# Optimization experiments

Measured on AMD Instinct MI355X. Metric: run time of the kernel, lower is better.

Reference implementation:

```python
import jax, jax.numpy as jnp
import numpy as np

NH = 8          # number of attention heads
RAND_P = 0.1    # random attention probability
EPS = 1e-5      # LayerNorm eps (torch default)


def _layer_norm(x, g, b):
    m = x.mean(-1, keepdims=True)
    v = ((x - m) ** 2).mean(-1, keepdims=True)
    return (x - m) * jax.lax.rsqrt(v + EPS) * g + b


def _make_mask(u, n_frames, spatial):
    # random(0/1) + tiled-eye position mask + block-diagonal frame mask (additive float mask)
    L = n_frames * spatial
    idx = jnp.arange(L)
    frame_id = idx // spatial
    pos_id = idx % spatial
    rand = (u >= RAND_P).astype(jnp.float32)
    pos = (pos_id[:, None] == pos_id[None, :]).astype(jnp.float32)
    frame = (frame_id[:, None] == frame_id[None, :]).astype(jnp.float32)
    return rand + pos + frame  # [L, L], values in {0,1,2,3}


def _attn_block(f, u, Wqkv, bqkv, Wo, bo, g1, b1, Wfc1, bfc1, Wfc2, bfc2, g2, b2):
    N, C, H, W = f.shape
    S = H * W
    L = N * S
    hd = C // NH
    src = f.transpose(0, 2, 3, 1).reshape(L, C)  # (n,h,w) flatten order, batch=1 squeezed
    mask = _make_mask(u, N, S)

    qkv = src @ Wqkv.T + bqkv                    # [L, 3C]
    q, k, v = jnp.split(qkv, 3, axis=-1)
    q = q.reshape(L, NH, hd).transpose(1, 0, 2) * (hd ** -0.5)  # [H, L, hd]
    k = k.reshape(L, NH, hd).transpose(1, 0, 2)
    v = v.reshape(L, NH, hd).transpose(1, 0, 2)

    scores = jnp.einsum('hqd,hkd->hqk', q, k) + mask[None]      # [H, L, L]
    attn = jax.nn.softmax(scores, axis=-1)
    o = jnp.einsum('hqk,hkd->hqd', attn, v).transpose(1, 0, 2).reshape(L, C)
    src2 = o @ Wo.T + bo

    x = _layer_norm(src + src2, g1, b1)          # residual + LN (dropout p=0 -> identity)
    h = jax.nn.relu(x @ Wfc1.T + bfc1)
    x = _layer_norm(x + h @ Wfc2.T + bfc2, g2, b2)
    return x.reshape(N, H, W, C).transpose(0, 3, 1, 2)


def setup_inputs() -> dict:
    key = jax.random.key(0)
    ks = jax.random.split(key, 12)
    D = 256
    s = 0.02
    return {
        'f0': jax.random.normal(ks[0], (2, D, 80, 80), jnp.float32),
        'f1': jax.random.normal(ks[1], (2, D, 40, 40), jnp.float32),
        'f2': jax.random.normal(ks[2], (2, D, 32, 32), jnp.float32),
        'f3': jax.random.normal(ks[3], (2, D, 16, 16), jnp.float32),
        'u2': jax.random.uniform(ks[4], (2048, 2048), jnp.float32),
        'u3': jax.random.uniform(ks[5], (512, 512), jnp.float32),
        'Wqkv': jax.random.normal(ks[6], (3 * D, D), jnp.float32) * s,
        'bqkv': jnp.zeros((3 * D,), jnp.float32),
        'Wo': jax.random.normal(ks[7], (D, D), jnp.float32) * s,
        'bo': jnp.zeros((D,), jnp.float32),
        'g1': jnp.ones((D,), jnp.float32),
        'b1': jnp.zeros((D,), jnp.float32),
        'Wfc1': jax.random.normal(ks[8], (4 * D, D), jnp.float32) * s,
        'bfc1': jnp.zeros((4 * D,), jnp.float32),
        'Wfc2': jax.random.normal(ks[9], (D, 4 * D), jnp.float32) * s,
        'bfc2': jnp.zeros((D,), jnp.float32),
        'g2': jnp.ones((D,), jnp.float32),
        'b2': jnp.zeros((D,), jnp.float32),
    }


def reference(f0, f1, f2, f3, u2, u3, Wqkv, bqkv, Wo, bo, g1, b1,
              Wfc1, bfc1, Wfc2, bfc2, g2, b2):
    params = (Wqkv, bqkv, Wo, bo, g1, b1, Wfc1, bfc1, Wfc2, bfc2, g2, b2)
    # levels 0 and 1 pass through untouched (loop starts at i=2)
    out2 = _attn_block(f2, u2, *params)
    out3 = _attn_block(f3, u3, *params)
    return (f0, f1, out2, out3)
```

## Files before the change

kernel.cpp:

```cpp
#include <hip/hip_runtime.h>
#include <hip/hip_bf16.h>
#include <cstddef>


typedef __attribute__((ext_vector_type(8))) short s16x8;
typedef __attribute__((ext_vector_type(4))) short s16x4;
typedef __attribute__((ext_vector_type(4))) float f32x4;
typedef __attribute__((ext_vector_type(2))) unsigned int u32x2;
typedef unsigned short ushort_t;
typedef unsigned long long u64;

#define RTOT 2560

__device__ inline unsigned short f2bf(float x) {
    union { __hip_bfloat16 h; unsigned short u; } cv;
    cv.h = __float2bfloat16(x);
    return cv.u;
}
__device__ inline float bf2f(unsigned short u) {
    union { unsigned int i; float f; } cv;
    cv.i = ((unsigned int)u) << 16;
    return cv.f;
}

__global__ __launch_bounds__(256) void prep(const float* __restrict__ f0,
                                            const float* __restrict__ f1,
                                            float* __restrict__ outp,
                                            const float* __restrict__ wqkv,
                                            const float* __restrict__ wo,
                                            const float* __restrict__ wfc1,
                                            const float* __restrict__ wfc2,
                                            ushort_t* __restrict__ o1,
                                            ushort_t* __restrict__ o2,
                                            ushort_t* __restrict__ o3,
                                            ushort_t* __restrict__ o4,
                                            const float* __restrict__ u2,
                                            const float* __restrict__ u3,
                                            u64* __restrict__ ub,
                                            const float* __restrict__ f2,
                                            const float* __restrict__ f3,
                                            float* __restrict__ srcf,
                                            ushort_t* __restrict__ srcb) {
    __shared__ float tl[64][65];
    int bid = blockIdx.x;
    int t = threadIdx.x;
    if (bid < 160) {
        int b = bid;
        const float* src; int S, rowb, n, ct, ht;
        if (b < 128) {
            n = b >> 6; int rem = b & 63; ct = rem >> 4; ht = rem & 15;
            src = f2; S = 1024; rowb = 0;
        } else {
            int b2 = b - 128;
            n = b2 >> 4; int rem = b2 & 15; ct = rem >> 2; ht = rem & 3;
            src = f3; S = 256; rowb = 2048;
        }
        int c0 = ct * 64, hw0 = ht * 64;
        int i = t >> 6, lane = t & 63;
#pragma unroll
        for (int jj = 0; jj < 16; ++jj) {
            int cl = i * 16 + jj;
            tl[lane][cl] = src[(size_t)(n * 256 + c0 + cl) * S + hw0 + lane];
        }
        __syncthreads();
#pragma unroll
        for (int jj = 0; jj < 16; ++jj) {
            int hl = i * 16 + jj;
            int row = rowb + n * S + hw0 + hl;
            float v = tl[hl][lane];
            srcf[(size_t)row * 256 + c0 + lane] = v;
            srcb[(size_t)row * 256 + c0 + lane] = f2bf(v);
        }
    } else if (bid < 4160) {
        int idx = (bid - 160) * 256 + t;
        f32x4 v = (idx < 819200) ? ((const f32x4*)f0)[idx]
                                 : ((const f32x4*)f1)[idx - 819200];
        ((f32x4*)outp)[idx] = v;
    } else if (bid < 4928) {
        int i = (bid - 4160) * 256 + t;
        const float* src; ushort_t* dst; int li;
        if (i < 49152)       { src = wqkv; dst = o1; li = i; }
        else if (i < 65536)  { src = wo;   dst = o2; li = i - 49152; }
        else if (i < 131072) { src = wfc1; dst = o3; li = i - 65536; }
        else                 { src = wfc2; dst = o4; li = i - 131072; }
        f32x4 v = ((const f32x4*)src)[li];
        s16x4 r;
        r[0] = (short)f2bf(v[0]); r[1] = (short)f2bf(v[1]);
        r[2] = (short)f2bf(v[2]); r[3] = (short)f2bf(v[3]);
        ((s16x4*)dst)[li] = r;
    } else {
        int gw = ((bid - 4928) * 256 + t) >> 6;
        int lane = t & 63;
        const float* p;
        u64* dst;
        if (gw < 16384) {
            int row = gw >> 3, ch = gw & 7;
            p = &u2[(size_t)row * 2048 + ch * 256 + lane * 4];
            dst = &ub[(size_t)gw * 4];
        } else {
            int lw = gw - 16384;
            int row = lw >> 1, ch = lw & 1;
            p = &u3[(size_t)row * 512 + ch * 256 + lane * 4];
            dst = &ub[65536 + (size_t)lw * 4];
        }
        f32x4 v = *(const f32x4*)p;
        u64 b0 = __ballot(v[0] >= 0.1f);
        u64 b1 = __ballot(v[1] >= 0.1f);
        u64 b2 = __ballot(v[2] >= 0.1f);
        u64 b3 = __ballot(v[3] >= 0.1f);
        if (lane < 4) {
            u64 bb = (lane == 0) ? b0 : (lane == 1) ? b1 : (lane == 2) ? b2 : b3;
            dst[lane] = bb;
        }
    }
}

#define ASTR 72

template <int EPI>
__global__ __launch_bounds__(256) void gemm64(const ushort_t* __restrict__ A,
                                              const ushort_t* __restrict__ W,
                                              const float* __restrict__ bias,
                                              ushort_t* __restrict__ outb,
                                              int M, int N, int K) {
    __shared__ __align__(16) ushort_t As[2][64 * ASTR];
    __shared__ __align__(16) ushort_t Ws[2][64 * ASTR];

    const int t = threadIdx.x;
    const int w = t >> 6, l = t & 63;
    const int c = l & 15, g = l >> 4;
    const int mh = w >> 1, nh = w & 1;
    const int m0 = blockIdx.y * 64, n0 = blockIdx.x * 64;
    const int srow = t >> 3;
    const int cg8 = (t & 7) * 8;

    const ushort_t* Aip0 = &A[(size_t)(m0 + srow) * K + cg8];
    const ushort_t* Aip1 = &A[(size_t)(m0 + 32 + srow) * K + cg8];
    const ushort_t* Wip0 = &W[(size_t)(n0 + srow) * K + cg8];
    const ushort_t* Wip1 = &W[(size_t)(n0 + 32 + srow) * K + cg8];

    s16x8 ra0 = *(const s16x8*)Aip0;
    s16x8 ra1 = *(const s16x8*)Aip1;
    s16x8 rw0 = *(const s16x8*)Wip0;
    s16x8 rw1 = *(const s16x8*)Wip1;
    *(s16x8*)&As[0][srow * ASTR + cg8] = ra0;
    *(s16x8*)&As[0][(32 + srow) * ASTR + cg8] = ra1;
    *(s16x8*)&Ws[0][srow * ASTR + cg8] = rw0;
    *(s16x8*)&Ws[0][(32 + srow) * ASTR + cg8] = rw1;
    __syncthreads();

    f32x4 acc[2][2] = {{{0.f,0.f,0.f,0.f},{0.f,0.f,0.f,0.f}},
                       {{0.f,0.f,0.f,0.f},{0.f,0.f,0.f,0.f}}};
    const int nsteps = K >> 6;

    for (int ks = 0; ks < nsteps; ++ks) {
        const int b = ks & 1;
        const bool pf = (ks + 1 < nsteps);
        if (pf) {
            int ko = (ks + 1) << 6;
            ra0 = *(const s16x8*)(Aip0 + ko);
            ra1 = *(const s16x8*)(Aip1 + ko);
            rw0 = *(const s16x8*)(Wip0 + ko);
            rw1 = *(const s16x8*)(Wip1 + ko);
        }
#pragma unroll
        for (int sl = 0; sl < 2; ++sl) {
            s16x8 af0 = *(const s16x8*)&As[b][(32 * mh + c) * ASTR + sl * 32 + 8 * g];
            s16x8 af1 = *(const s16x8*)&As[b][(32 * mh + 16 + c) * ASTR + sl * 32 + 8 * g];
            s16x8 wf0 = *(const s16x8*)&Ws[b][(32 * nh + c) * ASTR + sl * 32 + 8 * g];
            s16x8 wf1 = *(const s16x8*)&Ws[b][(32 * nh + 16 + c) * ASTR + sl * 32 + 8 * g];
            acc[0][0] = __builtin_amdgcn_mfma_f32_16x16x32_bf16(af0, wf0, acc[0][0], 0, 0, 0);
            acc[0][1] = __builtin_amdgcn_mfma_f32_16x16x32_bf16(af0, wf1, acc[0][1], 0, 0, 0);
            acc[1][0] = __builtin_amdgcn_mfma_f32_16x16x32_bf16(af1, wf0, acc[1][0], 0, 0, 0);
            acc[1][1] = __builtin_amdgcn_mfma_f32_16x16x32_bf16(af1, wf1, acc[1][1], 0, 0, 0);
        }
        if (pf) {
            int nb = b ^ 1;
            *(s16x8*)&As[nb][srow * ASTR + cg8] = ra0;
            *(s16x8*)&As[nb][(32 + srow) * ASTR + cg8] = ra1;
            *(s16x8*)&Ws[nb][srow * ASTR + cg8] = rw0;
            *(s16x8*)&Ws[nb][(32 + srow) * ASTR + cg8] = rw1;
        }
        __syncthreads();
    }

#pragma unroll
    for (int i = 0; i < 2; ++i)
#pragma unroll
    for (int j = 0; j < 2; ++j) {
        int n = n0 + 32 * nh + 16 * j + c;
        float bv = bias[n];
        float sc = 1.f;
        if (EPI == 3) sc = (n < 256) ? 0.17677669529663687f : 1.f;
#pragma unroll
        for (int r = 0; r < 4; ++r) {
            int m = m0 + 32 * mh + 16 * i + 4 * g + r;
            float v = acc[i][j][r] + bv;
            if (EPI == 1) v = fmaxf(v, 0.f);
            if (EPI == 3) v *= sc;
            outb[(size_t)m * N + n] = f2bf(v);
        }
    }
}

__global__ __launch_bounds__(128) void gemm_fc2(const ushort_t* __restrict__ A,
                                                const ushort_t* __restrict__ W,
                                                const float* __restrict__ bias,
                                                const float* __restrict__ res,
                                                float* __restrict__ outf,
                                                int M, int N, int K) {
    __shared__ __align__(16) ushort_t As[2][32 * ASTR];
    __shared__ __align__(16) ushort_t Ws[2][32 * ASTR];

    const int t = threadIdx.x;
    const int w = t >> 6, l = t & 63;
    const int c = l & 15, g = l >> 4;
    const int m0 = blockIdx.y * 32, n0 = blockIdx.x * 32;
    const int srow = t >> 3;
    const int cg8 = (t & 7) * 8;

    const ushort_t* Aip0 = &A[(size_t)(m0 + srow) * K + cg8];
    const ushort_t* Aip1 = &A[(size_t)(m0 + 16 + srow) * K + cg8];
    const ushort_t* Wip0 = &W[(size_t)(n0 + srow) * K + cg8];
    const ushort_t* Wip1 = &W[(size_t)(n0 + 16 + srow) * K + cg8];

    s16x8 ra0 = *(const s16x8*)Aip0;
    s16x8 ra1 = *(const s16x8*)Aip1;
    s16x8 rw0 = *(const s16x8*)Wip0;
    s16x8 rw1 = *(const s16x8*)Wip1;
    *(s16x8*)&As[0][srow * ASTR + cg8] = ra0;
    *(s16x8*)&As[0][(16 + srow) * ASTR + cg8] = ra1;
    *(s16x8*)&Ws[0][srow * ASTR + cg8] = rw0;
    *(s16x8*)&Ws[0][(16 + srow) * ASTR + cg8] = rw1;
    __syncthreads();

    f32x4 acc[2] = {{0.f, 0.f, 0.f, 0.f}, {0.f, 0.f, 0.f, 0.f}};
    const int nsteps = K >> 6;

    for (int ks = 0; ks < nsteps; ++ks) {
        const int b = ks & 1;
        const bool pf = (ks + 1 < nsteps);
        if (pf) {
            int ko = (ks + 1) << 6;
            ra0 = *(const s16x8*)(Aip0 + ko);
            ra1 = *(const s16x8*)(Aip1 + ko);
            rw0 = *(const s16x8*)(Wip0 + ko);
            rw1 = *(const s16x8*)(Wip1 + ko);
        }
#pragma unroll
        for (int kt = 0; kt < 2; ++kt) {
            s16x8 af = *(const s16x8*)&As[b][(16 * w + c) * ASTR + kt * 32 + 8 * g];
            s16x8 wf0 = *(const s16x8*)&Ws[b][c * ASTR + kt * 32 + 8 * g];
            s16x8 wf1 = *(const s16x8*)&Ws[b][(16 + c) * ASTR + kt * 32 + 8 * g];
            acc[0] = __builtin_amdgcn_mfma_f32_16x16x32_bf16(af, wf0, acc[0], 0, 0, 0);
            acc[1] = __builtin_amdgcn_mfma_f32_16x16x32_bf16(af, wf1, acc[1], 0, 0, 0);
        }
        if (pf) {
            int nb = b ^ 1;
            *(s16x8*)&As[nb][srow * ASTR + cg8] = ra0;
            *(s16x8*)&As[nb][(16 + srow) * ASTR + cg8] = ra1;
            *(s16x8*)&Ws[nb][srow * ASTR + cg8] = rw0;
            *(s16x8*)&Ws[nb][(16 + srow) * ASTR + cg8] = rw1;
        }
        __syncthreads();
    }

#pragma unroll
    for (int nt = 0; nt < 2; ++nt) {
        int n = n0 + 16 * nt + c;
        float bv = bias[n];
#pragma unroll
        for (int r = 0; r < 4; ++r) {
            int m = m0 + 16 * w + 4 * g + r;
            float v = acc[nt][r] + bv + res[(size_t)m * N + n];
            outf[(size_t)m * N + n] = v;
        }
    }
}

__global__ __launch_bounds__(128) void gemm_wo(const ushort_t* __restrict__ Opart,
                                               const float2* __restrict__ ml,
                                               const ushort_t* __restrict__ W,
                                               const float* __restrict__ bias,
                                               const float* __restrict__ res,
                                               float* __restrict__ outf) {
    const int K = 256, N = 256;
    __shared__ __align__(16) ushort_t As[2][32 * ASTR];
    __shared__ __align__(16) ushort_t Ws[2][32 * ASTR];

    const int t = threadIdx.x;
    const int w = t >> 6, l = t & 63;
    const int c = l & 15, g = l >> 4;
    const int m0 = blockIdx.y * 32, n0 = blockIdx.x * 32;
    const int srow = t >> 3;
    const int cg8 = (t & 7) * 8;

    auto loadA = [&](int row, int kcol) -> s16x8 {
        int head = kcol >> 5;
        float2 a0 = ml[((size_t)0 * RTOT + row) * 8 + head];
        float2 a1 = ml[((size_t)1 * RTOT + row) * 8 + head];
        float2 a2 = ml[((size_t)2 * RTOT + row) * 8 + head];
        float2 a3 = ml[((size_t)3 * RTOT + row) * 8 + head];
        float M = fmaxf(fmaxf(a0.x, a1.x), fmaxf(a2.x, a3.x));
        float w1 = __expf(a0.x - M), w2 = __expf(a1.x - M);
        float w3 = __expf(a2.x - M), w4 = __expf(a3.x - M);
        float inv = 1.f / (w1 * a0.y + w2 * a1.y + w3 * a2.y + w4 * a3.y);
        const size_t str = (size_t)RTOT * 256;
        size_t base = (size_t)row * 256 + kcol;
        s16x8 o1 = *(const s16x8*)&Opart[base];
        s16x8 o2 = *(const s16x8*)&Opart[base + str];
        s16x8 o3 = *(const s16x8*)&Opart[base + 2 * str];
        s16x8 o4 = *(const s16x8*)&Opart[base + 3 * str];
        s16x8 r;
#pragma unroll
        for (int e = 0; e < 8; ++e) {
            float v = w1 * bf2f((ushort_t)o1[e]) + w2 * bf2f((ushort_t)o2[e])
                    + w3 * bf2f((ushort_t)o3[e]) + w4 * bf2f((ushort_t)o4[e]);
            r[e] = (short)f2bf(v * inv);
        }
        return r;
    };

    const ushort_t* Wip0 = &W[(size_t)(n0 + srow) * K + cg8];
    const ushort_t* Wip1 = &W[(size_t)(n0 + 16 + srow) * K + cg8];

    s16x8 ra0 = loadA(m0 + srow, cg8);
    s16x8 ra1 = loadA(m0 + 16 + srow, cg8);
    s16x8 rw0 = *(const s16x8*)Wip0;
    s16x8 rw1 = *(const s16x8*)Wip1;
    *(s16x8*)&As[0][srow * ASTR + cg8] = ra0;
    *(s16x8*)&As[0][(16 + srow) * ASTR + cg8] = ra1;
    *(s16x8*)&Ws[0][srow * ASTR + cg8] = rw0;
    *(s16x8*)&Ws[0][(16 + srow) * ASTR + cg8] = rw1;
    __syncthreads();

    f32x4 acc[2] = {{0.f, 0.f, 0.f, 0.f}, {0.f, 0.f, 0.f, 0.f}};
    const int nsteps = 4;

    for (int ks = 0; ks < nsteps; ++ks) {
        const int b = ks & 1;
        const bool pf = (ks + 1 < nsteps);
        if (pf) {
            int ko = (ks + 1) << 6;
            ra0 = loadA(m0 + srow, ko + cg8);
            ra1 = loadA(m0 + 16 + srow, ko + cg8);
            rw0 = *(const s16x8*)(Wip0 + ko);
            rw1 = *(const s16x8*)(Wip1 + ko);
        }
#pragma unroll
        for (int kt = 0; kt < 2; ++kt) {
            s16x8 af = *(const s16x8*)&As[b][(16 * w + c) * ASTR + kt * 32 + 8 * g];
            s16x8 wf0 = *(const s16x8*)&Ws[b][c * ASTR + kt * 32 + 8 * g];
            s16x8 wf1 = *(const s16x8*)&Ws[b][(16 + c) * ASTR + kt * 32 + 8 * g];
            acc[0] = __builtin_amdgcn_mfma_f32_16x16x32_bf16(af, wf0, acc[0], 0, 0, 0);
            acc[1] = __builtin_amdgcn_mfma_f32_16x16x32_bf16(af, wf1, acc[1], 0, 0, 0);
        }
        if (pf) {
            int nb = b ^ 1;
            *(s16x8*)&As[nb][srow * ASTR + cg8] = ra0;
            *(s16x8*)&As[nb][(16 + srow) * ASTR + cg8] = ra1;
            *(s16x8*)&Ws[nb][srow * ASTR + cg8] = rw0;
            *(s16x8*)&Ws[nb][(16 + srow) * ASTR + cg8] = rw1;
        }
        __syncthreads();
    }

#pragma unroll
    for (int nt = 0; nt < 2; ++nt) {
        int n = n0 + 16 * nt + c;
        float bv = bias[n];
#pragma unroll
        for (int r = 0; r < 4; ++r) {
            int m = m0 + 16 * w + 4 * g + r;
            outf[(size_t)m * 256 + n] = acc[nt][r] + bv + res[(size_t)m * 256 + n];
        }
    }
}

#define KS 40
#define VS 66
#define PS 72
#define OS 68

__global__ __launch_bounds__(256) void flash_split(const ushort_t* __restrict__ qkvb,
                                                   const u64* __restrict__ ubits,
                                                   ushort_t* __restrict__ Opart,
                                                   float2* __restrict__ ml) {
    __shared__ __align__(16) ushort_t ks[2][64 * KS];
    __shared__ __align__(16) ushort_t vts[2][32 * VS];
    __shared__ __align__(16) char pso[64 * PS * 2];
    ushort_t* ps = (ushort_t*)pso;
    float* os = (float*)pso;

    const int bx = blockIdx.x;
    int qt, h, split, L, sshift, rowbase;
    const u64* ub;
    if (bx < 1024) {
        qt = bx & 31; h = (bx >> 5) & 7; split = bx >> 8;
        L = 2048; sshift = 10; rowbase = 0; ub = ubits;
    } else {
        int lo = bx - 1024;
        qt = lo & 7; h = (lo >> 3) & 7; split = lo >> 6;
        L = 512; sshift = 8; rowbase = 2048; ub = ubits + 65536;
    }
    const int tps = (L >> 6) >> 2;
    const int ts0 = split * tps;
    const int nch = L >> 8;

    const int t = threadIdx.x;
    const int w = t >> 6;
    const int l = t & 63;
    const int c = l & 15;
    const int g = l >> 4;
    const int smask = (1 << sshift) - 1;

    const int srow = t >> 2;
    const int sc8 = (t & 3) * 8;
    const int q0g = rowbase + qt * 64;

    const int ql = qt * 64 + 16 * w + c;
    const s16x8 qf = *(const s16x8*)&qkvb[(size_t)(rowbase + ql) * 768 + h * 32 + 8 * g];
    const int qp = ql & smask, qfr = ql >> sshift;
    const u64* ubq = &ub[(size_t)ql * nch * 4];

    s16x8 kreg, vreg;
    {
        size_t base = (size_t)(rowbase + ts0 * 64 + srow) * 768 + h * 32 + sc8;
        s16x8 k0r = *(const s16x8*)&qkvb[base + 256];
        s16x8 v0r = *(const s16x8*)&qkvb[base + 512];
        *(s16x8*)&ks[0][srow * KS + sc8] = k0r;
#pragma unroll
        for (int i = 0; i < 8; ++i)
            vts[0][(sc8 + i) * VS + srow] = (ushort_t)v0r[i];
        if (tps > 1) {
            kreg = *(const s16x8*)&qkvb[base + 64 * 768 + 256];
            vreg = *(const s16x8*)&qkvb[base + 64 * 768 + 512];
        }
    }
    __syncthreads();

    f32x4 oacc0 = {0.f, 0.f, 0.f, 0.f};
    f32x4 oacc1 = {0.f, 0.f, 0.f, 0.f};
    float mold = -3e38f, lrun = 0.f;
    const f32x4 zc = {0.f, 0.f, 0.f, 0.f};

    u64 wr0 = 0, wr1 = 0, wr2 = 0, wr3 = 0;
    int cur = 0;
    for (int kt = 0; kt < tps; ++kt) {
        const int nxt = cur ^ 1;
        const int gt = ts0 + kt;
        const int k0 = gt << 6;

        if (kt + 1 < tps) {
            *(s16x8*)&ks[nxt][srow * KS + sc8] = kreg;
#pragma unroll
            for (int i = 0; i < 8; ++i)
                vts[nxt][(sc8 + i) * VS + srow] = (ushort_t)vreg[i];
        }
        if (kt + 2 < tps) {
            size_t base = (size_t)(rowbase + (gt + 2) * 64 + srow) * 768 + h * 32 + sc8;
            kreg = *(const s16x8*)&qkvb[base + 256];
            vreg = *(const s16x8*)&qkvb[base + 512];
        }

        if ((gt & 3) == 0 || kt == 0) {
            const u64* bp = &ubq[(size_t)(gt >> 2) * 4];
            wr0 = bp[0]; wr1 = bp[1]; wr2 = bp[2]; wr3 = bp[3];
        }
        const unsigned shb = 16 * (gt & 3);

        f32x4 sacc[4];
#pragma unroll
        for (int nt = 0; nt < 4; ++nt) {
            s16x8 kf = *(const s16x8*)&ks[cur][(16 * nt + c) * KS + 8 * g];
            sacc[nt] = __builtin_amdgcn_mfma_f32_16x16x32_bf16(kf, qf, zc, 0, 0, 0);
        }

        float sv[4][4];
        float m = -3e38f;
#pragma unroll
        for (int nt = 0; nt < 4; ++nt) {
            unsigned sh = shb + 4 * nt + g;
#pragma unroll
            for (int r = 0; r < 4; ++r) {
                u64 wrd = (r == 0) ? wr0 : (r == 1) ? wr1 : (r == 2) ? wr2 : wr3;
                int kg = k0 + 16 * nt + 4 * g + r;
                float s = sacc[nt][r]
                        + ((wrd >> sh) & 1 ? 1.f : 0.f)
                        + ((kg & smask) == qp ? 1.f : 0.f)
                        + ((kg >> sshift) == qfr ? 1.f : 0.f);
                sv[nt][r] = s;
                m = fmaxf(m, s);
            }
        }
        m = fmaxf(m, __shfl_xor(m, 16));
        m = fmaxf(m, __shfl_xor(m, 32));
        float newm = fmaxf(mold, m);
        float fac = __expf(mold - newm);
        mold = newm;

        float sum = 0.f;
#pragma unroll
        for (int nt = 0; nt < 4; ++nt) {
            float p0 = __expf(sv[nt][0] - newm);
            float p1 = __expf(sv[nt][1] - newm);
            float p2 = __expf(sv[nt][2] - newm);
            float p3 = __expf(sv[nt][3] - newm);
            sum += (p0 + p1) + (p2 + p3);
            u32x2 pk;
            pk[0] = ((unsigned)f2bf(p1) << 16) | f2bf(p0);
            pk[1] = ((unsigned)f2bf(p3) << 16) | f2bf(p2);
            *(u32x2*)&ps[(16 * w + c) * PS + 16 * nt + 4 * g] = pk;
        }
        sum += __shfl_xor(sum, 16);
        sum += __shfl_xor(sum, 32);
        lrun = lrun * fac + sum;
        oacc0 *= fac;
        oacc1 *= fac;

#pragma unroll
        for (int kc = 0; kc < 2; ++kc) {
            s16x8 pfr = *(const s16x8*)&ps[(16 * w + c) * PS + 32 * kc + 8 * g];
            s16x8 vf0 = *(const s16x8*)&vts[cur][c * VS + 32 * kc + 8 * g];
            s16x8 vf1 = *(const s16x8*)&vts[cur][(16 + c) * VS + 32 * kc + 8 * g];
            oacc0 = __builtin_amdgcn_mfma_f32_16x16x32_bf16(vf0, pfr, oacc0, 0, 0, 0);
            oacc1 = __builtin_amdgcn_mfma_f32_16x16x32_bf16(vf1, pfr, oacc1, 0, 0, 0);
        }

        __syncthreads();
        cur = nxt;
    }

    if (g == 0) {
        int q = q0g + 16 * w + c;
        ml[((size_t)split * RTOT + q) * 8 + h] = make_float2(mold, lrun);
    }

#pragma unroll
    for (int r = 0; r < 4; ++r) {
        os[(4 * g + r) * OS + 16 * w + c] = oacc0[r];
        os[(16 + 4 * g + r) * OS + 16 * w + c] = oacc1[r];
    }
    __syncthreads();
    {
        int r = t >> 2, d0 = (t & 3) * 8;
        s16x8 pk;
#pragma unroll
        for (int i = 0; i < 8; ++i) pk[i] = (short)f2bf(os[(d0 + i) * OS + r]);
        *(s16x8*)&Opart[((size_t)split * RTOT + q0g + r) * 256 + h * 32 + d0] = pk;
    }
}

__global__ __launch_bounds__(256) void ln1_kernel(const float* __restrict__ in,
                                                  const float* __restrict__ g,
                                                  const float* __restrict__ b,
                                                  float* __restrict__ outf,
                                                  ushort_t* __restrict__ outb) {
    __shared__ float red[256];
    int row = blockIdx.x, t = threadIdx.x;
    float v = in[(size_t)row * 256 + t];
    red[t] = v;
    __syncthreads();
    for (int s = 128; s > 0; s >>= 1) {
        if (t < s) red[t] += red[t + s];
        __syncthreads();
    }
    float mean = red[0] * (1.f / 256.f);
    __syncthreads();
    float d = v - mean;
    red[t] = d * d;
    __syncthreads();
    for (int s = 128; s > 0; s >>= 1) {
        if (t < s) red[t] += red[t + s];
        __syncthreads();
    }
    float var = red[0] * (1.f / 256.f);
    float r = d * rsqrtf(var + 1e-5f) * g[t] + b[t];
    outf[(size_t)row * 256 + t] = r;
    outb[(size_t)row * 256 + t] = f2bf(r);
}

__global__ __launch_bounds__(256) void ln2_out(const float* __restrict__ in,
                                               const float* __restrict__ g,
                                               const float* __restrict__ b,
                                               float* __restrict__ out2,
                                               float* __restrict__ out3) {
    __shared__ float red[256];
    int row = blockIdx.x, t = threadIdx.x;
    float v = in[(size_t)row * 256 + t];
    red[t] = v;
    __syncthreads();
    for (int s = 128; s > 0; s >>= 1) {
        if (t < s) red[t] += red[t + s];
        __syncthreads();
    }
    float mean = red[0] * (1.f / 256.f);
    __syncthreads();
    float d = v - mean;
    red[t] = d * d;
    __syncthreads();
    for (int s = 128; s > 0; s >>= 1) {
        if (t < s) red[t] += red[t + s];
        __syncthreads();
    }
    float var = red[0] * (1.f / 256.f);
    float r = d * rsqrtf(var + 1e-5f) * g[t] + b[t];
    if (row < 2048) {
        int n = row >> 10, hw = row & 1023;
        out2[((size_t)(n * 256 + t) << 10) + hw] = r;
    } else {
        int rl = row - 2048;
        int n = rl >> 8, hw = rl & 255;
        out3[((size_t)(n * 256 + t) << 8) + hw] = r;
    }
}


extern "C" void kernel_launch(void* const* d_in, const int* in_sizes, int n_in,
                              void* d_out, int out_size, void* d_ws, size_t ws_size,
                              hipStream_t stream) {
    const float* f0 = (const float*)d_in[0];
    const float* f1 = (const float*)d_in[1];
    const float* f2 = (const float*)d_in[2];
    const float* f3 = (const float*)d_in[3];
    const float* u2 = (const float*)d_in[4];
    const float* u3 = (const float*)d_in[5];
    const float* Wqkv = (const float*)d_in[6];
    const float* bqkv = (const float*)d_in[7];
    const float* Wo   = (const float*)d_in[8];
    const float* bo   = (const float*)d_in[9];
    const float* g1   = (const float*)d_in[10];
    const float* b1   = (const float*)d_in[11];
    const float* Wfc1 = (const float*)d_in[12];
    const float* bfc1 = (const float*)d_in[13];
    const float* Wfc2 = (const float*)d_in[14];
    const float* bfc2 = (const float*)d_in[15];
    const float* g2   = (const float*)d_in[16];
    const float* b2   = (const float*)d_in[17];

    float* out = (float*)d_out;
    float* ws = (float*)d_ws;

    ushort_t* wqkv = (ushort_t*)ws;
    ushort_t* wo   = (ushort_t*)(ws + 98304);
    ushort_t* wfc1 = (ushort_t*)(ws + 131072);
    ushort_t* wfc2 = (ushort_t*)(ws + 262144);

    float* sc = ws + 393216;
    float*    src_f32 = sc;
    ushort_t* qkvb    = (ushort_t*)(sc + 655360);
    ushort_t* src_bf  = (ushort_t*)(sc + 1638400);
    float*    t1      = sc + 1966080;
    float*    x_f32   = sc + 2621440;
    u64*      ubits   = (u64*)x_f32;
    ushort_t* x_bf    = (ushort_t*)(sc + 3276800);
    float2*   ml      = (float2*)(sc + 3604480);
    ushort_t* Opart   = (ushort_t*)(sc + 3768320);
    ushort_t* h_bf    = Opart;

    prep<<<9280, 256, 0, stream>>>(f0, f1, out,
                                   Wqkv, Wo, Wfc1, Wfc2, wqkv, wo, wfc1, wfc2,
                                   u2, u3, ubits, f2, f3, src_f32, src_bf);

    gemm64<3><<<dim3(12, 40), 256, 0, stream>>>(
        src_bf, wqkv, bqkv, qkvb, RTOT, 768, 256);
    flash_split<<<1280, 256, 0, stream>>>(qkvb, ubits, Opart, ml);
    gemm_wo<<<dim3(8, 80), 128, 0, stream>>>(Opart, ml, wo, bo, src_f32, t1);
    ln1_kernel<<<2560, 256, 0, stream>>>(t1, g1, b1, x_f32, x_bf);
    gemm64<1><<<dim3(16, 40), 256, 0, stream>>>(
        x_bf, wfc1, bfc1, h_bf, RTOT, 1024, 256);
    gemm_fc2<<<dim3(8, 80), 128, 0, stream>>>(
        h_bf, wfc2, bfc2, x_f32, t1, RTOT, 256, 1024);
    ln2_out<<<2560, 256, 0, stream>>>(t1, g2, b2, out + 4096000, out + 4620288);
}
```

Measured before the change: 90.49 us.

## Split-K the Wo and FC2 GEMMs in two, summing partials in LayerNorm

The output-projection and FC2 GEMMs are each launched with a second grid dimension. Each half computes half of the K reduction and writes its partial result to a separate buffer. Only the first half adds bias and residual, and the following LayerNorm kernels sum the two partials as they load. This doubles the block count of two small GEMMs to fill more compute units, at the cost of extra partial-sum traffic and a reshuffled workspace layout.

```diff
diff --git a/kernel.cpp b/kernel.cpp
--- a/kernel.cpp
+++ b/kernel.cpp
@@ -11,6 +11,7 @@
 typedef unsigned long long u64;
 
 #define RTOT 2560
+#define HALF 655360
 
 __device__ inline unsigned short f2bf(float x) {
     union { __hip_bfloat16 h; unsigned short u; } cv;
@@ -216,13 +217,15 @@
     const int w = t >> 6, l = t & 63;
     const int c = l & 15, g = l >> 4;
     const int m0 = blockIdx.y * 32, n0 = blockIdx.x * 32;
+    const int z = blockIdx.z;
+    const int koff = z * (K >> 1);
     const int srow = t >> 3;
     const int cg8 = (t & 7) * 8;
 
-    const ushort_t* Aip0 = &A[(size_t)(m0 + srow) * K + cg8];
-    const ushort_t* Aip1 = &A[(size_t)(m0 + 16 + srow) * K + cg8];
-    const ushort_t* Wip0 = &W[(size_t)(n0 + srow) * K + cg8];
-    const ushort_t* Wip1 = &W[(size_t)(n0 + 16 + srow) * K + cg8];
+    const ushort_t* Aip0 = &A[(size_t)(m0 + srow) * K + koff + cg8];
+    const ushort_t* Aip1 = &A[(size_t)(m0 + 16 + srow) * K + koff + cg8];
+    const ushort_t* Wip0 = &W[(size_t)(n0 + srow) * K + koff + cg8];
+    const ushort_t* Wip1 = &W[(size_t)(n0 + 16 + srow) * K + koff + cg8];
 
     s16x8 ra0 = *(const s16x8*)Aip0;
     s16x8 ra1 = *(const s16x8*)Aip1;
@@ -235,7 +238,7 @@
     __syncthreads();
 
     f32x4 acc[2] = {{0.f, 0.f, 0.f, 0.f}, {0.f, 0.f, 0.f, 0.f}};
-    const int nsteps = K >> 6;
+    const int nsteps = K >> 7;
 
     for (int ks = 0; ks < nsteps; ++ks) {
         const int b = ks & 1;
@@ -265,15 +268,17 @@
         __syncthreads();
     }
 
+    float* op = outf + (size_t)z * HALF;
 #pragma unroll
     for (int nt = 0; nt < 2; ++nt) {
         int n = n0 + 16 * nt + c;
-        float bv = bias[n];
+        float bv = (z == 0) ? bias[n] : 0.f;
 #pragma unroll
         for (int r = 0; r < 4; ++r) {
             int m = m0 + 16 * w + 4 * g + r;
-            float v = acc[nt][r] + bv + res[(size_t)m * N + n];
-            outf[(size_t)m * N + n] = v;
+            float v = acc[nt][r] + bv;
+            if (z == 0) v += res[(size_t)m * N + n];
+            op[(size_t)m * N + n] = v;
         }
     }
 }
@@ -292,6 +297,8 @@
     const int w = t >> 6, l = t & 63;
     const int c = l & 15, g = l >> 4;
     const int m0 = blockIdx.y * 32, n0 = blockIdx.x * 32;
+    const int z = blockIdx.z;
+    const int koff = z * 128;
     const int srow = t >> 3;
     const int cg8 = (t & 7) * 8;
 
@@ -321,11 +328,11 @@
         return r;
     };
 
-    const ushort_t* Wip0 = &W[(size_t)(n0 + srow) * K + cg8];
-    const ushort_t* Wip1 = &W[(size_t)(n0 + 16 + srow) * K + cg8];
-
-    s16x8 ra0 = loadA(m0 + srow, cg8);
-    s16x8 ra1 = loadA(m0 + 16 + srow, cg8);
+    const ushort_t* Wip0 = &W[(size_t)(n0 + srow) * K + koff + cg8];
+    const ushort_t* Wip1 = &W[(size_t)(n0 + 16 + srow) * K + koff + cg8];
+
+    s16x8 ra0 = loadA(m0 + srow, koff + cg8);
+    s16x8 ra1 = loadA(m0 + 16 + srow, koff + cg8);
     s16x8 rw0 = *(const s16x8*)Wip0;
     s16x8 rw1 = *(const s16x8*)Wip1;
     *(s16x8*)&As[0][srow * ASTR + cg8] = ra0;
@@ -335,15 +342,15 @@
     __syncthreads();
 
     f32x4 acc[2] = {{0.f, 0.f, 0.f, 0.f}, {0.f, 0.f, 0.f, 0.f}};
-    const int nsteps = 4;
+    const int nsteps = 2;
 
     for (int ks = 0; ks < nsteps; ++ks) {
         const int b = ks & 1;
         const bool pf = (ks + 1 < nsteps);
         if (pf) {
             int ko = (ks + 1) << 6;
-            ra0 = loadA(m0 + srow, ko + cg8);
-            ra1 = loadA(m0 + 16 + srow, ko + cg8);
+            ra0 = loadA(m0 + srow, koff + ko + cg8);
+            ra1 = loadA(m0 + 16 + srow, koff + ko + cg8);
             rw0 = *(const s16x8*)(Wip0 + ko);
             rw1 = *(const s16x8*)(Wip1 + ko);
         }
@@ -365,14 +372,17 @@
         __syncthreads();
     }
 
+    float* op = outf + (size_t)z * HALF;
 #pragma unroll
     for (int nt = 0; nt < 2; ++nt) {
         int n = n0 + 16 * nt + c;
-        float bv = bias[n];
+        float bv = (z == 0) ? bias[n] : 0.f;
 #pragma unroll
         for (int r = 0; r < 4; ++r) {
             int m = m0 + 16 * w + 4 * g + r;
-            outf[(size_t)m * 256 + n] = acc[nt][r] + bv + res[(size_t)m * 256 + n];
+            float v = acc[nt][r] + bv;
+            if (z == 0) v += res[(size_t)m * 256 + n];
+            op[(size_t)m * 256 + n] = v;
         }
     }
 }
@@ -558,7 +568,8 @@
                                                   ushort_t* __restrict__ outb) {
     __shared__ float red[256];
     int row = blockIdx.x, t = threadIdx.x;
-    float v = in[(size_t)row * 256 + t];
+    size_t idx = (size_t)row * 256 + t;
+    float v = in[idx] + in[idx + HALF];
     red[t] = v;
     __syncthreads();
     for (int s = 128; s > 0; s >>= 1) {
@@ -576,8 +587,8 @@
     }
     float var = red[0] * (1.f / 256.f);
     float r = d * rsqrtf(var + 1e-5f) * g[t] + b[t];
-    outf[(size_t)row * 256 + t] = r;
-    outb[(size_t)row * 256 + t] = f2bf(r);
+    outf[idx] = r;
+    outb[idx] = f2bf(r);
 }
 
 __global__ __launch_bounds__(256) void ln2_out(const float* __restrict__ in,
@@ -587,7 +598,8 @@
                                                float* __restrict__ out3) {
     __shared__ float red[256];
     int row = blockIdx.x, t = threadIdx.x;
-    float v = in[(size_t)row * 256 + t];
+    size_t idx = (size_t)row * 256 + t;
+    float v = in[idx] + in[idx + HALF];
     red[t] = v;
     __syncthreads();
     for (int s = 128; s > 0; s >>= 1) {
@@ -651,12 +663,13 @@
     ushort_t* qkvb    = (ushort_t*)(sc + 655360);
     ushort_t* src_bf  = (ushort_t*)(sc + 1638400);
     float*    t1      = sc + 1966080;
-    float*    x_f32   = sc + 2621440;
+    float*    x_f32   = sc + 3276800;
     u64*      ubits   = (u64*)x_f32;
-    ushort_t* x_bf    = (ushort_t*)(sc + 3276800);
-    float2*   ml      = (float2*)(sc + 3604480);
-    ushort_t* Opart   = (ushort_t*)(sc + 3768320);
+    ushort_t* x_bf    = (ushort_t*)(sc + 3932160);
+    float2*   ml      = (float2*)(sc + 4259840);
+    ushort_t* Opart   = (ushort_t*)(sc + 4423680);
     ushort_t* h_bf    = Opart;
+    float*    t2      = sc + 5734400;
 
     prep<<<9280, 256, 0, stream>>>(f0, f1, out,
                                    Wqkv, Wo, Wfc1, Wfc2, wqkv, wo, wfc1, wfc2,
@@ -665,11 +678,11 @@
     gemm64<3><<<dim3(12, 40), 256, 0, stream>>>(
         src_bf, wqkv, bqkv, qkvb, RTOT, 768, 256);
     flash_split<<<1280, 256, 0, stream>>>(qkvb, ubits, Opart, ml);
-    gemm_wo<<<dim3(8, 80), 128, 0, stream>>>(Opart, ml, wo, bo, src_f32, t1);
+    gemm_wo<<<dim3(8, 80, 2), 128, 0, stream>>>(Opart, ml, wo, bo, src_f32, t1);
     ln1_kernel<<<2560, 256, 0, stream>>>(t1, g1, b1, x_f32, x_bf);
     gemm64<1><<<dim3(16, 40), 256, 0, stream>>>(
         x_bf, wfc1, bfc1, h_bf, RTOT, 1024, 256);
-    gemm_fc2<<<dim3(8, 80), 128, 0, stream>>>(
-        h_bf, wfc2, bfc2, x_f32, t1, RTOT, 256, 1024);
-    ln2_out<<<2560, 256, 0, stream>>>(t1, g2, b2, out + 4096000, out + 4620288);
-}
+    gemm_fc2<<<dim3(8, 80, 2), 128, 0, stream>>>(
+        h_bf, wfc2, bfc2, x_f32, t2, RTOT, 256, 1024);
+    ln2_out<<<2560, 256, 0, stream>>>(t2, g2, b2, out + 4096000, out + 4620288);
+}
```

Result: no change. 91.84 us (+1.5%).
